# Optimization experiments

Measured on AMD Instinct MI355X. Metric: run time of the kernel, lower is better.

Reference implementation:

```python
import jax, jax.numpy as jnp
import numpy as np
from jax import lax

B, S, C, D, V = 256, 50, 40, 256, 20000
T_DIFF = 1000
BETA_START, BETA_END = 1e-4, 2e-2


def _lstm(x, Wih, Whh, bih, bhh):
    # x: [B,S,D]; single-layer LSTM, batch_first, eval mode (no dropout)
    Bb = x.shape[0]
    H = Whh.shape[1]
    def step(carry, xt):
        h, c = carry
        g = xt @ Wih.T + bih + h @ Whh.T + bhh  # [B,4H]
        i, f, gg, o = jnp.split(g, 4, axis=-1)
        i = jax.nn.sigmoid(i); f = jax.nn.sigmoid(f)
        gg = jnp.tanh(gg); o = jax.nn.sigmoid(o)
        c = f * c + i * gg
        h = o * jnp.tanh(c)
        return (h, c), h
    h0 = jnp.zeros((Bb, H), x.dtype)
    (_, _), hs = lax.scan(step, (h0, h0), x.transpose(1, 0, 2))
    return hs.transpose(1, 0, 2)  # [B,S,H]


def setup_inputs() -> dict:
    key = jax.random.key(0)
    ks = jax.random.split(key, 20)
    sc = 0.05
    inp = {
        'input_seqs': jax.random.randint(ks[0], (B, S, C), 0, V),
        'masks': jnp.zeros((B, S), jnp.int32),
        'lengths': jax.random.randint(ks[1], (B,), 1, S + 1),
        'seq_time_step': jax.random.uniform(ks[2], (B, S), jnp.float32),
        'code_masks': jnp.zeros((B, S, C), jnp.int32),
        'diffusion_time_t': jax.random.randint(ks[3], (B,), 0, T_DIFF),
        'normal_noise': jax.random.normal(ks[4], (B, S, D), jnp.float32),
        # learned parameters
        'emb': jax.random.normal(ks[5], (V + 1, D), jnp.float32) * sc,
        'Wih': jax.random.normal(ks[6], (4 * D, D), jnp.float32) * sc,
        'Whh': jax.random.normal(ks[7], (4 * D, D), jnp.float32) * sc,
        'bih': jnp.zeros((4 * D,), jnp.float32),
        'bhh': jnp.zeros((4 * D,), jnp.float32),
        'Whk': jax.random.normal(ks[8], (D, D), jnp.float32) * sc,
        'bhk': jnp.zeros((D,), jnp.float32),
        'W1': jax.random.normal(ks[9], (64, 2 * D), jnp.float32) * sc,
        'b1': jnp.zeros((64,), jnp.float32),
        'W2': jax.random.normal(ks[10], (2, 64), jnp.float32) * sc,
        'b2': jnp.zeros((2,), jnp.float32),
        'Wdiff': jax.random.normal(ks[11], (D, D), jnp.float32) * sc,
        'bdiff': jnp.zeros((D,), jnp.float32),
        'temb': jax.random.normal(ks[12], (T_DIFF, D), jnp.float32) * sc,
        'Wout': jax.random.normal(ks[13], (2, D), jnp.float32) * sc,
        'bout': jnp.zeros((2,), jnp.float32),
    }
    # padding_idx row zeroed like nn.Embedding(padding_idx=-1)
    inp['emb'] = inp['emb'].at[V].set(0.0)
    return inp


def reference(input_seqs, masks, lengths, seq_time_step, code_masks,
              diffusion_time_t, normal_noise,
              emb, Wih, Whh, bih, bhh, Whk, bhk, W1, b1, W2, b2,
              Wdiff, bdiff, temb, Wout, bout):
    # embedding sum over codes per visit
    x = emb[input_seqs].sum(axis=2)  # [B,S,D]
    rnn_out = _lstm(x, Wih, Whh, bih, bhh)  # [B,S,D]

    # vectorized alignment loop: e_k is ALWAYS x[:,0] (as in source),
    # position i>=1 attends between e_k and w_hk(rnn_out[i-1])
    w = rnn_out @ Whk.T + bhk  # [B,S,D]
    e_k = x[:, :1, :]  # [B,1,D]
    wprev = w[:, :-1, :]  # [B,S-1,D] -> timestep i uses w[i-1]
    cat = jnp.concatenate([jnp.broadcast_to(e_k, wprev.shape), wprev], -1)
    attn = jax.nn.softmax(jnp.tanh(cat @ W1.T + b1) @ W2.T + b2, axis=-1)  # [B,S-1,2]
    aligned_rest = e_k * attn[..., 0:1] + wprev * attn[..., 1:2]
    aligned_e_t = jnp.concatenate([e_k, aligned_rest], axis=1)  # [B,S,D]

    # diffusion noising (linear beta schedule as in ehr.yml defaults)
    betas = jnp.linspace(BETA_START, BETA_END, T_DIFF, dtype=jnp.float32)
    alpha = jnp.cumprod(1.0 - betas)[diffusion_time_t][:, None, None]
    noisy = aligned_e_t * jnp.sqrt(alpha) + normal_noise * jnp.sqrt(1.0 - alpha)

    # UNet surrogate (source unavailable): timestep-conditioned linear map
    predicted_noise = (noisy + temb[diffusion_time_t][:, None, :]) @ Wdiff + bdiff

    gen_x = aligned_e_t + (normal_noise - predicted_noise)
    pool_x = jnp.max(x, axis=1) @ Wout.T + bout  # [B,2]
    gen_pool_x = jnp.max(gen_x, axis=1) @ Wout.T + bout  # [B,2]
    return (pool_x, gen_pool_x, predicted_noise, normal_noise)
```

## Files before the change

### kernel.cpp

```cpp
#include <hip/hip_runtime.h>
#include <cmath>

#define Bb 256
#define Ss 50
#define Cc 40
#define Dd 256
#define Vv 20000

typedef __bf16 bf16;
typedef __bf16 bf16x8 __attribute__((ext_vector_type(8)));
typedef float f32x4 __attribute__((ext_vector_type(4)));
typedef unsigned long long u64;

#define GL2LDS(g, l) __builtin_amdgcn_global_load_lds( \
    (__attribute__((address_space(1))) void*)(g), \
    (__attribute__((address_space(3))) void*)(l), 16, 0, 0)

#define OFFB_GATES    0ull
#define OFFB_ALIGNED  0ull
#define OFFB_WBB      13107200ull
#define OFFB_TMPB     25952256ull
#define OFFB_H1       32505856ull
#define OFFB_X        52428800ull
#define OFFB_XB       65536000ull
#define OFFB_RNNB     72089600ull
#define OFFB_W        78643200ull
#define OFFB_BAR      91750400ull
#define OFFB_WIHB     92012544ull
#define OFFB_WHHB     92536832ull
#define OFFB_WHKB     93061120ull
#define OFFB_W1B      93192192ull
#define OFFB_WDTB     93257728ull
#define OFFB_SALPHA   93388800ull
#define OFFB_SBETA    93389824ull

template<int BM, int BN, int ACT>
__global__ __launch_bounds__(256) void mfma_gemm(
    const bf16* __restrict__ A, int lda,
    const bf16* __restrict__ B, int ldb,
    const float* __restrict__ bias1, const float* __restrict__ bias2,
    float* __restrict__ C, bf16* __restrict__ Cb, int ldc, int K)
{
    constexpr int BK = 32;
    constexpr int NF = BN / 32;
    __shared__ bf16 As[BM * BK];
    __shared__ bf16 Bs[BN * BK];
    const int tid  = threadIdx.x;
    const int wave = tid >> 6;
    const int lane = tid & 63;
    const int m0 = blockIdx.x * BM;
    const int n0 = blockIdx.y * BN;
    const int wm = (wave >> 1) * 64;
    const int wn = (wave & 1) * (BN / 2);

    f32x4 acc[4][NF];
#pragma unroll
    for (int i = 0; i < 4; ++i)
#pragma unroll
        for (int j = 0; j < NF; ++j) acc[i][j] = (f32x4){0.f, 0.f, 0.f, 0.f};

    const int ar = tid >> 2;
    const int ac = tid & 3;
    const int sw = ac ^ (ar & 3);
    const int lr = lane & 15;
    const int q  = lane >> 4;

    for (int k0 = 0; k0 < K; k0 += BK) {
        __syncthreads();
#pragma unroll
        for (int it = 0; it < BM / 64; ++it) {
            const bf16* gp = A + (size_t)(m0 + it * 64 + ar) * lda + k0 + sw * 8;
            GL2LDS(gp, As + it * 2048 + wave * 512);
        }
#pragma unroll
        for (int it = 0; it < BN / 64; ++it) {
            const bf16* gp = B + (size_t)(n0 + it * 64 + ar) * ldb + k0 + sw * 8;
            GL2LDS(gp, Bs + it * 2048 + wave * 512);
        }
        __syncthreads();

        bf16x8 af[4], bfv[NF];
#pragma unroll
        for (int fm = 0; fm < 4; ++fm) {
            int m = wm + fm * 16 + lr;
            af[fm] = *(const bf16x8*)(As + m * 32 + ((q ^ (m & 3)) * 8));
        }
#pragma unroll
        for (int fn = 0; fn < NF; ++fn) {
            int n = wn + fn * 16 + lr;
            bfv[fn] = *(const bf16x8*)(Bs + n * 32 + ((q ^ (n & 3)) * 8));
        }
#pragma unroll
        for (int fm = 0; fm < 4; ++fm)
#pragma unroll
            for (int fn = 0; fn < NF; ++fn)
                acc[fm][fn] = __builtin_amdgcn_mfma_f32_16x16x32_bf16(
                    af[fm], bfv[fn], acc[fm][fn], 0, 0, 0);
    }

    const int rbase = q * 4;
#pragma unroll
    for (int fn = 0; fn < NF; ++fn) {
        const int col = n0 + wn + fn * 16 + lr;
        float bb = 0.f;
        if (bias1) bb += bias1[col];
        if (bias2) bb += bias2[col];
#pragma unroll
        for (int fm = 0; fm < 4; ++fm) {
            f32x4 v = acc[fm][fn];
#pragma unroll
            for (int r = 0; r < 4; ++r) {
                const int row = m0 + wm + fm * 16 + rbase + r;
                float val = v[r] + bb;
                if (ACT == 1) val = tanhf(val);
                C[(size_t)row * ldc + col] = val;
                if (Cb) Cb[(size_t)row * ldc + col] = (bf16)val;
            }
        }
    }
}

__global__ __launch_bounds__(256) void h1_gemm(
    const bf16* __restrict__ xb, const bf16* __restrict__ wbb,
    const bf16* __restrict__ W1b,
    const float* __restrict__ b1, float* __restrict__ H1)
{
    constexpr int BM = 128, BN = 64, BK = 32, NF = 2;
    constexpr int K = 512;
    __shared__ bf16 As[BM * BK];
    __shared__ bf16 Bs[BN * BK];
    const int tid  = threadIdx.x;
    const int wave = tid >> 6;
    const int lane = tid & 63;
    const int m0 = blockIdx.x * BM;
    const int wm = (wave >> 1) * 64;
    const int wn = (wave & 1) * 32;

    f32x4 acc[4][NF];
#pragma unroll
    for (int i = 0; i < 4; ++i)
#pragma unroll
        for (int j = 0; j < NF; ++j) acc[i][j] = (f32x4){0.f, 0.f, 0.f, 0.f};

    const int ar = tid >> 2;
    const int ac = tid & 3;
    const int sw = ac ^ (ar & 3);
    const int lr = lane & 15;
    const int q  = lane >> 4;

    for (int k0 = 0; k0 < K; k0 += BK) {
        __syncthreads();
#pragma unroll
        for (int it = 0; it < 2; ++it) {
            const int row = m0 + it * 64 + ar;
            const int b = row / (Ss - 1), t = row - b * (Ss - 1);
            const int col = k0 + sw * 8;
            const bf16* gp = (col < 256)
                ? xb  + (size_t)b * (Ss * Dd) + col
                : wbb + ((size_t)(b * Ss + t)) * Dd + (col - 256);
            GL2LDS(gp, As + it * 2048 + wave * 512);
        }
        {
            const bf16* gp = W1b + (size_t)ar * K + k0 + sw * 8;
            GL2LDS(gp, Bs + wave * 512);
        }
        __syncthreads();

        bf16x8 af[4], bfv[NF];
#pragma unroll
        for (int fm = 0; fm < 4; ++fm) {
            int m = wm + fm * 16 + lr;
            af[fm] = *(const bf16x8*)(As + m * 32 + ((q ^ (m & 3)) * 8));
        }
#pragma unroll
        for (int fn = 0; fn < NF; ++fn) {
            int n = wn + fn * 16 + lr;
            bfv[fn] = *(const bf16x8*)(Bs + n * 32 + ((q ^ (n & 3)) * 8));
        }
#pragma unroll
        for (int fm = 0; fm < 4; ++fm)
#pragma unroll
            for (int fn = 0; fn < NF; ++fn)
                acc[fm][fn] = __builtin_amdgcn_mfma_f32_16x16x32_bf16(
                    af[fm], bfv[fn], acc[fm][fn], 0, 0, 0);
    }

    const int rbase = q * 4;
#pragma unroll
    for (int fn = 0; fn < NF; ++fn) {
        const int col = wn + fn * 16 + lr;
        const float bb = b1[col];
#pragma unroll
        for (int fm = 0; fm < 4; ++fm) {
            f32x4 v = acc[fm][fn];
#pragma unroll
            for (int r = 0; r < 4; ++r) {
                const int row = m0 + wm + fm * 16 + rbase + r;
                H1[(size_t)row * 64 + col] = tanhf(v[r] + bb);
            }
        }
    }
}

__global__ __launch_bounds__(512, 2) void lstm_quad(
    const bf16* __restrict__ Whhb,
    const float* __restrict__ gates,
    bf16* __restrict__ rnnb,
    unsigned* __restrict__ bar)
{
    __shared__ bf16 hb0[16 * 256];
    __shared__ bf16 hb1[16 * 256];
    __shared__ float pacc[4][4][16][17];
    const int tid  = threadIdx.x;
    const int w    = tid >> 6;
    const int lane = tid & 63;
    const int lr   = lane & 15;
    const int q    = lane >> 4;
    const int bm   = blockIdx.x & 15;
    const int bd   = blockIdx.x >> 4;
    const int kh   = w >> 2;
    const int ct   = w & 3;
    const int dg   = bd * 64 + ct * 16 + lr;

    f32x4 wfr[4][4];
#pragma unroll
    for (int g = 0; g < 4; ++g) {
        const bf16* brow = Whhb + (size_t)(g * 256 + dg) * Dd + kh * 128 + q * 8;
#pragma unroll
        for (int kc = 0; kc < 4; ++kc)
            wfr[g][kc] = *(const f32x4*)(brow + kc * 32);
    }

    const float* gp[4];
#pragma unroll
    for (int r = 0; r < 4; ++r)
        gp[r] = gates + (size_t)(bm * 16 + q * 4 + r) * (Ss * 1024) + dg;

    const int xrow = tid >> 4, xc8 = tid & 15;
    const size_t my_base = ((size_t)(bm * 16 + xrow) * Ss) * Dd + bd * 64 + xc8 * 4;
    const int pack_off = xrow * 512 + (((bd * 8 + (xc8 >> 1)) ^ (xrow & 7)) << 4) + (xc8 & 1) * 8;

    const int pA  = tid >> 8;
    const int pdA = pA + (pA >= bd ? 1 : 0);
    const int pdB = 2 + (2 >= bd ? 1 : 0);
    const int rowA = (tid >> 4) & 15, xqA = tid & 15;
    const size_t gA = ((size_t)(bm * 16 + rowA) * Ss) * Dd + pdA * 64 + xqA * 4;
    const size_t gB = ((size_t)(bm * 16 + xrow) * Ss) * Dd + pdB * 64 + xc8 * 4;
    const int unpA = rowA * 512 + (((pdA * 8 + (xqA >> 1)) ^ (rowA & 7)) << 4) + (xqA & 1) * 8;
    const int unpB = xrow * 512 + (((pdB * 8 + (xc8 >> 1)) ^ (xrow & 7)) << 4) + (xc8 & 1) * 8;
    unsigned* myf = bar + (bm * 4 + bd) * 32;
    unsigned* pfA = bar + (bm * 4 + pdA) * 32;
    unsigned* pfB = bar + (bm * 4 + pdB) * 32;

    int ew_off[4];
#pragma unroll
    for (int r = 0; r < 4; ++r) {
        const int row = q * 4 + r;
        ew_off[r] = row * 512 + (((dg >> 3) ^ (row & 7)) << 4) + (dg & 7) * 2;
    }

    float c[4] = {0.f, 0.f, 0.f, 0.f};
    float gaA[4][4], gaB[4][4];
    if (kh == 0) {
#pragma unroll
        for (int r = 0; r < 4; ++r)
#pragma unroll
            for (int g = 0; g < 4; ++g) gaA[g][r] = gp[r][g * 256];
    }

#define STEP(T, GACUR, GANEXT, RD, WR, FIRST)                                   \
    {                                                                           \
        f32x4 acc[4];                                                           \
        _Pragma("unroll")                                                       \
        for (int g = 0; g < 4; ++g) acc[g] = (f32x4){0.f, 0.f, 0.f, 0.f};       \
        if (!(FIRST)) {                                                         \
            bf16x8 af[4];                                                       \
            _Pragma("unroll")                                                   \
            for (int kc = 0; kc < 4; ++kc)                                      \
                af[kc] = *(const bf16x8*)((const char*)(RD) + lr * 512          \
                         + (((kh * 16 + kc * 4 + q) ^ (lr & 7)) << 4));         \
            _Pragma("unroll")                                                   \
            for (int kc = 0; kc < 4; ++kc)                                      \
                _Pragma("unroll")                                               \
                for (int g = 0; g < 4; ++g)                                     \
                    acc[g] = __builtin_amdgcn_mfma_f32_16x16x32_bf16(           \
                        af[kc], __builtin_bit_cast(bf16x8, wfr[g][kc]),         \
                        acc[g], 0, 0, 0);                                       \
        }                                                                       \
        if (kh == 1) {                                                          \
            _Pragma("unroll")                                                   \
            for (int g = 0; g < 4; ++g)                                         \
                _Pragma("unroll")                                               \
                for (int r = 0; r < 4; ++r)                                     \
                    pacc[ct][g][q * 4 + r][lr] = acc[g][r];                     \
        }                                                                       \
        __syncthreads();                          \
        if (kh == 0) {                                                          \
            _Pragma("unroll")                                                   \
            for (int r = 0; r < 4; ++r) {                                       \
                float gi = acc[0][r] + pacc[ct][0][q * 4 + r][lr] + GACUR[0][r];\
                float gf = acc[1][r] + pacc[ct][1][q * 4 + r][lr] + GACUR[1][r];\
                float gg = acc[2][r] + pacc[ct][2][q * 4 + r][lr] + GACUR[2][r];\
                float go = acc[3][r] + pacc[ct][3][q * 4 + r][lr] + GACUR[3][r];\
                float ii  = 1.f / (1.f + expf(-gi));                            \
                float ff  = 1.f / (1.f + expf(-gf));                            \
                float g2t = tanhf(gg);                                          \
                float oo  = 1.f / (1.f + expf(-go));                            \
                c[r] = ff * c[r] + ii * g2t;                                    \
                *(bf16*)((char*)(WR) + ew_off[r]) = (bf16)(oo * tanhf(c[r]));   \
            }                                                                   \
        }                                                                       \
        __syncthreads();                          \
        if (tid < 256) {                                                        \
            u64 v = *(const u64*)((const char*)(WR) + pack_off);                \
            __hip_atomic_store((u64*)(rnnb + my_base + (size_t)(T) * Dd), v,    \
                               __ATOMIC_RELAXED, __HIP_MEMORY_SCOPE_AGENT);     \
        }                                                                       \
        if ((T) != Ss - 1) {                                                    \
            __syncthreads();        \
            if (tid == 0)                                                       \
                __hip_atomic_store(myf, (unsigned)((T) + 1),                    \
                                   __ATOMIC_RELAXED, __HIP_MEMORY_SCOPE_AGENT); \
            if (kh == 0) {            \
                _Pragma("unroll")                                               \
                for (int r = 0; r < 4; ++r)                                     \
                    _Pragma("unroll")                                           \
                    for (int g = 0; g < 4; ++g)                                 \
                        GANEXT[g][r] = gp[r][(size_t)((T) + 1) * 1024 + g * 256];\
            }                                                                   \
            while (__hip_atomic_load(pfA, __ATOMIC_RELAXED,                     \
                                     __HIP_MEMORY_SCOPE_AGENT)                  \
                   < (unsigned)((T) + 1)) {}                                    \
            {                                                                   \
                u64 rv = __hip_atomic_load(                                     \
                    (const u64*)(rnnb + gA + (size_t)(T) * Dd),                 \
                    __ATOMIC_RELAXED, __HIP_MEMORY_SCOPE_AGENT);                \
                *(u64*)((char*)(WR) + unpA) = rv;                               \
            }                                                                   \
            if (tid < 256) {                                                    \
                while (__hip_atomic_load(pfB, __ATOMIC_RELAXED,                 \
                                         __HIP_MEMORY_SCOPE_AGENT)              \
                       < (unsigned)((T) + 1)) {}                                \
                u64 rv = __hip_atomic_load(                                     \
                    (const u64*)(rnnb + gB + (size_t)(T) * Dd),                 \
                    __ATOMIC_RELAXED, __HIP_MEMORY_SCOPE_AGENT);                \
                *(u64*)((char*)(WR) + unpB) = rv;                               \
            }                                                                   \
            __syncthreads();           \
        }                                                                       \
    }

    for (int t2 = 0; t2 < Ss; t2 += 2) {
        STEP(t2,     gaA, gaB, hb1, hb0, (t2 == 0));
        STEP(t2 + 1, gaB, gaA, hb0, hb1, false);
    }
#undef STEP
}

__global__ __launch_bounds__(256) void prep_kernel(
    const float* __restrict__ Wih, bf16* __restrict__ Wihb,
    const float* __restrict__ Whh, bf16* __restrict__ Whhb,
    const float* __restrict__ Whk, bf16* __restrict__ Whkb,
    const float* __restrict__ W1,  bf16* __restrict__ W1b,
    const float* __restrict__ Wdiff, bf16* __restrict__ WdTb,
    const int* __restrict__ tdiff, float* __restrict__ salpha,
    float* __restrict__ sbeta, unsigned* __restrict__ bar)
{
    __shared__ float t[32][33];
    int bx = blockIdx.x;
    const int tid = threadIdx.x;
    if (bx < 1024) { int i = bx * 256 + tid; Wihb[i] = (bf16)Wih[i]; return; }
    bx -= 1024;
    if (bx < 1024) { int i = bx * 256 + tid; Whhb[i] = (bf16)Whh[i]; return; }
    bx -= 1024;
    if (bx < 256)  { int i = bx * 256 + tid; Whkb[i] = (bf16)Whk[i]; return; }
    bx -= 256;
    if (bx < 128)  { int i = bx * 256 + tid; W1b[i]  = (bf16)W1[i];  return; }
    bx -= 128;
    if (bx < 64) {
        const int c0 = (bx & 7) * 32, r0 = (bx >> 3) * 32;
        const int tx = tid & 31, ty = tid >> 5;
        for (int i = ty; i < 32; i += 8)
            t[i][tx] = Wdiff[(size_t)(r0 + i) * 256 + c0 + tx];
        __syncthreads();
        for (int i = ty; i < 32; i += 8)
            WdTb[(size_t)(c0 + i) * 256 + r0 + tx] = (bf16)t[tx][i];
        return;
    }
#pragma unroll
    for (int j = 0; j < 8; ++j) bar[tid * 8 + j] = 0u;
    const int tt = tdiff[tid];
    const float step = (0.02f - 1e-4f) / 999.f;
    float prod = 1.f;
    for (int j = 0; j <= tt; ++j) prod *= (1.f - (1e-4f + j * step));
    salpha[tid] = sqrtf(prod);
    sbeta[tid]  = sqrtf(fmaxf(1.f - prod, 0.f));
}

__global__ __launch_bounds__(256) void embed_kernel(
    const int* __restrict__ seqs, const float* __restrict__ emb,
    float* __restrict__ x, bf16* __restrict__ xb)
{
    __shared__ int idx[Cc];
    const int bs = blockIdx.x;
    const int tid = threadIdx.x;
    if (tid < Cc) idx[tid] = seqs[(size_t)bs * Cc + tid];
    __syncthreads();
    float s = 0.f;
#pragma unroll 8
    for (int c = 0; c < Cc; ++c) s += emb[(size_t)idx[c] * Dd + tid];
    x[(size_t)bs * Dd + tid]  = s;
    xb[(size_t)bs * Dd + tid] = (bf16)s;
}

__global__ __launch_bounds__(256) void attn_diff_kernel(
    const float* __restrict__ x, const float* __restrict__ w,
    const float* __restrict__ H1, const float* __restrict__ W2,
    const float* __restrict__ b2, const float* __restrict__ noise,
    const float* __restrict__ temb, const int* __restrict__ tdiff,
    const float* __restrict__ salpha, const float* __restrict__ sbeta,
    float* __restrict__ aligned, bf16* __restrict__ tmpb,
    float* __restrict__ noise_out)
{
    __shared__ float sa[2];
    const int bs = blockIdx.x;
    const int b = bs / Ss, s = bs % Ss;
    const int d = threadIdx.x;
    if (s > 0 && threadIdx.x < 64) {
        const int r = b * (Ss - 1) + (s - 1);
        const int j = threadIdx.x;
        float h = H1[(size_t)r * 64 + j];
        float v0 = h * W2[j];
        float v1 = h * W2[64 + j];
#pragma unroll
        for (int off = 32; off; off >>= 1) { v0 += __shfl_down(v0, off); v1 += __shfl_down(v1, off); }
        if (j == 0) {
            float z0 = v0 + b2[0], z1 = v1 + b2[1];
            float m = fmaxf(z0, z1);
            float e0 = expf(z0 - m), e1 = expf(z1 - m);
            float inv = 1.f / (e0 + e1);
            sa[0] = e0 * inv;
            sa[1] = e1 * inv;
        }
    }
    __syncthreads();
    const float ek = x[((size_t)b * Ss) * Dd + d];
    float v;
    if (s == 0) {
        v = ek;
    } else {
        v = ek * sa[0] + w[((size_t)b * Ss + s - 1) * Dd + d] * sa[1];
    }
    const size_t i = (size_t)bs * Dd + d;
    aligned[i] = v;
    const int t = tdiff[b];
    tmpb[i] = (bf16)(v * salpha[b] + noise[i] * sbeta[b] + temb[(size_t)t * Dd + d]);
    noise_out[i] = noise[i];
}

__device__ inline void pool_reduce_write(float m, const float* __restrict__ Wout,
                                         const float* __restrict__ bout,
                                         float* __restrict__ outp, int b,
                                         float* r0, float* r1)
{
    float v0 = m * Wout[threadIdx.x];
    float v1 = m * Wout[Dd + threadIdx.x];
#pragma unroll
    for (int off = 32; off; off >>= 1) { v0 += __shfl_down(v0, off); v1 += __shfl_down(v1, off); }
    const int lane = threadIdx.x & 63, wv = threadIdx.x >> 6;
    if (lane == 0) { r0[wv] = v0; r1[wv] = v1; }
    __syncthreads();
    if (threadIdx.x == 0) {
        outp[b * 2 + 0] = r0[0] + r0[1] + r0[2] + r0[3] + bout[0];
        outp[b * 2 + 1] = r1[0] + r1[1] + r1[2] + r1[3] + bout[1];
    }
}

__global__ __launch_bounds__(256) void pool_x_kernel(
    const float* __restrict__ x, const float* __restrict__ Wout,
    const float* __restrict__ bout, float* __restrict__ outp)
{
    __shared__ float r0[4], r1[4];
    const int b = blockIdx.x, d = threadIdx.x;
    float m = -INFINITY;
    for (int s = 0; s < Ss; ++s) m = fmaxf(m, x[((size_t)b * Ss + s) * Dd + d]);
    pool_reduce_write(m, Wout, bout, outp, b, r0, r1);
}

__global__ __launch_bounds__(256) void gen_pool_kernel(
    const float* __restrict__ aligned, const float* __restrict__ noise,
    const float* __restrict__ pred, const float* __restrict__ Wout,
    const float* __restrict__ bout, float* __restrict__ outp)
{
    __shared__ float r0[4], r1[4];
    const int b = blockIdx.x, d = threadIdx.x;
    float m = -INFINITY;
    for (int s = 0; s < Ss; ++s) {
        const size_t i = ((size_t)b * Ss + s) * Dd + d;
        m = fmaxf(m, aligned[i] + noise[i] - pred[i]);
    }
    pool_reduce_write(m, Wout, bout, outp, b, r0, r1);
}

extern "C" void kernel_launch(void* const* d_in, const int* in_sizes, int n_in,
                              void* d_out, int out_size, void* d_ws, size_t ws_size,
                              hipStream_t stream)
{
    const int*   seqs  = (const int*)d_in[0];
    const int*   tdiff = (const int*)d_in[5];
    const float* noise = (const float*)d_in[6];
    const float* emb   = (const float*)d_in[7];
    const float* Wih   = (const float*)d_in[8];
    const float* Whh   = (const float*)d_in[9];
    const float* bih   = (const float*)d_in[10];
    const float* bhh   = (const float*)d_in[11];
    const float* Whk   = (const float*)d_in[12];
    const float* bhk   = (const float*)d_in[13];
    const float* W1    = (const float*)d_in[14];
    const float* b1    = (const float*)d_in[15];
    const float* W2    = (const float*)d_in[16];
    const float* b2    = (const float*)d_in[17];
    const float* Wdiff = (const float*)d_in[18];
    const float* bdiff = (const float*)d_in[19];
    const float* temb  = (const float*)d_in[20];
    const float* Wout  = (const float*)d_in[21];
    const float* bout  = (const float*)d_in[22];

    float* outp = (float*)d_out;
    char*  wsb  = (char*)d_ws;

    float* gates   = (float*)(wsb + OFFB_GATES);
    float* aligned = (float*)(wsb + OFFB_ALIGNED);
    bf16*  wbb     = (bf16*) (wsb + OFFB_WBB);
    bf16*  tmpb    = (bf16*) (wsb + OFFB_TMPB);
    float* H1      = (float*)(wsb + OFFB_H1);
    float* x       = (float*)(wsb + OFFB_X);
    bf16*  xb      = (bf16*) (wsb + OFFB_XB);
    bf16*  rnnb    = (bf16*) (wsb + OFFB_RNNB);
    float* wbuf    = (float*)(wsb + OFFB_W);
    unsigned* bar  = (unsigned*)(wsb + OFFB_BAR);
    bf16*  Wihb    = (bf16*) (wsb + OFFB_WIHB);
    bf16*  Whhb    = (bf16*) (wsb + OFFB_WHHB);
    bf16*  Whkb    = (bf16*) (wsb + OFFB_WHKB);
    bf16*  W1b     = (bf16*) (wsb + OFFB_W1B);
    bf16*  WdTb    = (bf16*) (wsb + OFFB_WDTB);
    float* salpha  = (float*)(wsb + OFFB_SALPHA);
    float* sbeta   = (float*)(wsb + OFFB_SBETA);

    float* pred_out  = outp + 1024;
    float* noise_out = outp + 1024 + (size_t)Bb * Ss * Dd;

    prep_kernel<<<2497, 256, 0, stream>>>(Wih, Wihb, Whh, Whhb, Whk, Whkb,
                                          W1, W1b, Wdiff, WdTb,
                                          tdiff, salpha, sbeta, bar);

    embed_kernel<<<Bb * Ss, 256, 0, stream>>>(seqs, emb, x, xb);

    pool_x_kernel<<<Bb, 256, 0, stream>>>(x, Wout, bout, outp);

    mfma_gemm<128, 128, 0><<<dim3(100, 8), 256, 0, stream>>>(
        xb, 256, Wihb, 256, bih, bhh, gates, nullptr, 1024, 256);

    lstm_quad<<<64, 512, 0, stream>>>(Whhb, gates, rnnb, bar);

    mfma_gemm<128, 128, 0><<<dim3(100, 2), 256, 0, stream>>>(
        rnnb, 256, Whkb, 256, bhk, nullptr, wbuf, wbb, 256, 256);

    h1_gemm<<<dim3(98, 1), 256, 0, stream>>>(xb, wbb, W1b, b1, H1);

    attn_diff_kernel<<<Bb * Ss, 256, 0, stream>>>(
        x, wbuf, H1, W2, b2, noise, temb, tdiff, salpha, sbeta,
        aligned, tmpb, noise_out);

    mfma_gemm<128, 128, 0><<<dim3(100, 2), 256, 0, stream>>>(
        tmpb, 256, WdTb, 256, bdiff, nullptr, pred_out, nullptr, 256, 256);

    gen_pool_kernel<<<Bb, 256, 0, stream>>>(aligned, noise, pred_out, Wout, bout, outp + 512);
}
```

Measured before the change: 480.4 us.

## Use per-wave step flags in LSTM exchange and vectorize embedding gather

In the persistent LSTM kernel, each of the four writer waves now publishes its own step flag right after its hidden-state stores drain. Readers poll only the flag covering the rows they need. This removes a block-wide barrier and the single-thread flag publish from every timestep's critical path. Separately, the embedding kernel now processes four tokens per block using float4 loads and stores, cutting launch count and raising bytes per load. The flag change relies on s_waitcnt plus relaxed atomics for ordering, which is subtle.

```diff
diff --git a/kernel.cpp b/kernel.cpp
--- a/kernel.cpp
+++ b/kernel.cpp
@@ -248,9 +248,9 @@
     const size_t gB = ((size_t)(bm * 16 + xrow) * Ss) * Dd + pdB * 64 + xc8 * 4;
     const int unpA = rowA * 512 + (((pdA * 8 + (xqA >> 1)) ^ (rowA & 7)) << 4) + (xqA & 1) * 8;
     const int unpB = xrow * 512 + (((pdB * 8 + (xc8 >> 1)) ^ (xrow & 7)) << 4) + (xc8 & 1) * 8;
-    unsigned* myf = bar + (bm * 4 + bd) * 32;
-    unsigned* pfA = bar + (bm * 4 + pdA) * 32;
-    unsigned* pfB = bar + (bm * 4 + pdB) * 32;
+    unsigned* myfw = bar + (bm * 4 + bd) * 32;
+    unsigned* pfAw = bar + (bm * 4 + pdA) * 32 + (rowA >> 2) * 8;
+    unsigned* pfBw = bar + (bm * 4 + pdB) * 32 + (xrow >> 2) * 8;
 
     int ew_off[4];
 #pragma unroll
@@ -311,16 +311,17 @@
             }                                                                   \
         }                                                                       \
         __syncthreads();                          \
-        if (tid < 256) {                                                        \
+        if (tid < 256) {        \
             u64 v = *(const u64*)((const char*)(WR) + pack_off);                \
             __hip_atomic_store((u64*)(rnnb + my_base + (size_t)(T) * Dd), v,    \
                                __ATOMIC_RELAXED, __HIP_MEMORY_SCOPE_AGENT);     \
+            asm volatile("s_waitcnt vmcnt(0)" ::: "memory");                    \
+            if ((tid & 63) == 0)                                                \
+                __hip_atomic_store(myfw + (tid >> 6) * 8,                       \
+                                   (unsigned)((T) + 1),                         \
+                                   __ATOMIC_RELAXED, __HIP_MEMORY_SCOPE_AGENT); \
         }                                                                       \
         if ((T) != Ss - 1) {                                                    \
-            __syncthreads();        \
-            if (tid == 0)                                                       \
-                __hip_atomic_store(myf, (unsigned)((T) + 1),                    \
-                                   __ATOMIC_RELAXED, __HIP_MEMORY_SCOPE_AGENT); \
             if (kh == 0) {            \
                 _Pragma("unroll")                                               \
                 for (int r = 0; r < 4; ++r)                                     \
@@ -328,7 +329,7 @@
                     for (int g = 0; g < 4; ++g)                                 \
                         GANEXT[g][r] = gp[r][(size_t)((T) + 1) * 1024 + g * 256];\
             }                                                                   \
-            while (__hip_atomic_load(pfA, __ATOMIC_RELAXED,                     \
+            while (__hip_atomic_load(pfAw, __ATOMIC_RELAXED,                    \
                                      __HIP_MEMORY_SCOPE_AGENT)                  \
                    < (unsigned)((T) + 1)) {}                                    \
             {                                                                   \
@@ -338,7 +339,7 @@
                 *(u64*)((char*)(WR) + unpA) = rv;                               \
             }                                                                   \
             if (tid < 256) {                                                    \
-                while (__hip_atomic_load(pfB, __ATOMIC_RELAXED,                 \
+                while (__hip_atomic_load(pfBw, __ATOMIC_RELAXED,                \
                                          __HIP_MEMORY_SCOPE_AGENT)              \
                        < (unsigned)((T) + 1)) {}                                \
                 u64 rv = __hip_atomic_load(                                     \
@@ -401,16 +402,20 @@
     const int* __restrict__ seqs, const float* __restrict__ emb,
     float* __restrict__ x, bf16* __restrict__ xb)
 {
-    __shared__ int idx[Cc];
-    const int bs = blockIdx.x;
+    __shared__ int idx[4][Cc];
     const int tid = threadIdx.x;
-    if (tid < Cc) idx[tid] = seqs[(size_t)bs * Cc + tid];
+    const int w = tid >> 6, l = tid & 63;
+    const int bs0 = blockIdx.x * 4;
+    if (tid < 4 * Cc) idx[tid / Cc][tid % Cc] = seqs[(size_t)bs0 * Cc + tid];
     __syncthreads();
-    float s = 0.f;
+    f32x4 s = (f32x4){0.f, 0.f, 0.f, 0.f};
 #pragma unroll 8
-    for (int c = 0; c < Cc; ++c) s += emb[(size_t)idx[c] * Dd + tid];
-    x[(size_t)bs * Dd + tid]  = s;
-    xb[(size_t)bs * Dd + tid] = (bf16)s;
+    for (int c = 0; c < Cc; ++c)
+        s += *(const f32x4*)(emb + (size_t)idx[w][c] * Dd + l * 4);
+    const size_t o = (size_t)(bs0 + w) * Dd + l * 4;
+    *(f32x4*)(x + o) = s;
+    bf16 b4[4] = {(bf16)s[0], (bf16)s[1], (bf16)s[2], (bf16)s[3]};
+    *(u64*)(xb + o) = *(const u64*)b4;
 }
 
 __global__ __launch_bounds__(256) void attn_diff_kernel(
@@ -554,7 +559,7 @@
                                           W1, W1b, Wdiff, WdTb,
                                           tdiff, salpha, sbeta, bar);
 
-    embed_kernel<<<Bb * Ss, 256, 0, stream>>>(seqs, emb, x, xb);
+    embed_kernel<<<(Bb * Ss) / 4, 256, 0, stream>>>(seqs, emb, x, xb);
 
     pool_x_kernel<<<Bb, 256, 0, stream>>>(x, Wout, bout, outp);
 
```

After: 511.0 us. +6.4%, slower.
